# Kernel tuning notes

Measured on AMD Instinct MI355X. Metric: run time of the kernel, lower is better.

## Reference

```python
import jax, jax.numpy as jnp
import numpy as np

B, S, I, H = 32, 1024, 256, 256
NUM_LAYERS = 2


def _lstm_dir(x, m, h0, c0, Wih, Whh, bih, bhh, reverse=False):
    """x: [S,B,in], m: [S,B,1]. Returns outs [S,B,H], hT, cT.
    PyTorch LSTMCell gate order: i, f, g, o. Masked reset to init state per step."""
    if reverse:
        x = x[::-1]
        m = m[::-1]

    def step(carry, xm):
        h, c = carry
        xt, mt = xm
        gates = xt @ Wih.T + bih + h @ Whh.T + bhh  # [B,4H]
        i, f, g, o = jnp.split(gates, 4, axis=-1)
        i = jax.nn.sigmoid(i)
        f = jax.nn.sigmoid(f)
        g = jnp.tanh(g)
        o = jax.nn.sigmoid(o)
        cn = f * c + i * g
        hn = o * jnp.tanh(cn)
        hn = hn * mt + h0 * (1.0 - mt)
        cn = cn * mt + c0 * (1.0 - mt)
        return (hn, cn), hn

    (hT, cT), outs = jax.lax.scan(step, (h0, c0), (x, m))
    if reverse:
        outs = outs[::-1]
    return outs, hT, cT


def setup_inputs() -> dict:
    key = jax.random.key(0)
    ks = iter(jax.random.split(key, 40))
    d = {
        "inputs": jax.random.normal(next(ks), (B, S, I), dtype=jnp.float32),
        "mask": jnp.ones((B, S), dtype=jnp.float32),
    }
    scale = 0.05
    for li in range(NUM_LAYERS):
        in_sz = I if li == 0 else 2 * H
        for d_tag in ("f", "b"):
            p = f"l{li}{d_tag}_"
            d[p + "Wih"] = jax.random.normal(next(ks), (4 * H, in_sz), dtype=jnp.float32) * scale
            d[p + "Whh"] = jax.random.normal(next(ks), (4 * H, H), dtype=jnp.float32) * scale
            d[p + "bih"] = jnp.zeros((4 * H,), dtype=jnp.float32)
            d[p + "bhh"] = jnp.zeros((4 * H,), dtype=jnp.float32)
    return d


def reference(inputs, mask,
              l0f_Wih, l0f_Whh, l0f_bih, l0f_bhh,
              l0b_Wih, l0b_Whh, l0b_bih, l0b_bhh,
              l1f_Wih, l1f_Whh, l1f_bih, l1f_bhh,
              l1b_Wih, l1b_Whh, l1b_bih, l1b_bhh):
    # batch_first -> time-major
    x = jnp.transpose(inputs, (1, 0, 2))          # [S,B,I]
    m = jnp.transpose(mask, (1, 0))[:, :, None]   # [S,B,1] broadcasts over H
    h0 = jnp.zeros((B, H), dtype=inputs.dtype)
    c0 = h0

    layers = [
        ((l0f_Wih, l0f_Whh, l0f_bih, l0f_bhh), (l0b_Wih, l0b_Whh, l0b_bih, l0b_bhh)),
        ((l1f_Wih, l1f_Whh, l1f_bih, l1f_bhh), (l1b_Wih, l1b_Whh, l1b_bih, l1b_bhh)),
    ]
    hn, cn = [], []
    for fw_p, bw_p in layers:
        # (dropout between layers only active in training mode; eval reference skips it)
        fw_out, fh, fc = _lstm_dir(x, m, h0, c0, *fw_p, reverse=False)
        bw_out, bh, bc = _lstm_dir(x, m, h0, c0, *bw_p, reverse=True)
        x = jnp.concatenate((fw_out, bw_out), axis=2)  # [S,B,2H]
        hn.append(jnp.concatenate((fh, bh), axis=1))
        cn.append(jnp.concatenate((fc, bc), axis=1))

    output = jnp.transpose(x, (1, 0, 2))  # [B,S,2H]
    return output, jnp.stack(hn, axis=0), jnp.stack(cn, axis=0)
```

## Files before the change

### kernel.cpp

```cpp
#include <hip/hip_runtime.h>
#include <cstddef>

typedef __attribute__((ext_vector_type(8))) short short8;
typedef __attribute__((ext_vector_type(4))) short short4v;
typedef __attribute__((ext_vector_type(4))) float f32x4;

__device__ __forceinline__ unsigned short f2bf(float f){
  unsigned u = __builtin_bit_cast(unsigned, f);
  u += 0x7FFFu + ((u >> 16) & 1u);
  return (unsigned short)(u >> 16);
}
__device__ __forceinline__ float bf2f(unsigned short h){
  unsigned u = ((unsigned)h) << 16;
  return __builtin_bit_cast(float, u);
}
__device__ __forceinline__ float sigf(float x){
  return __builtin_amdgcn_rcpf(1.0f + __builtin_amdgcn_exp2f(-1.4426950408889634f * x));
}
__device__ __forceinline__ float tanhf_(float x){
  return 1.0f - 2.0f * __builtin_amdgcn_rcpf(1.0f + __builtin_amdgcn_exp2f(2.8853900817779268f * x));
}

__global__ __launch_bounds__(64) void cast_x(const float* __restrict__ in, unsigned short* __restrict__ xb){
  int blk = blockIdx.x;
  int t = blk & 1023, b = blk >> 10;
  int k = threadIdx.x * 4;
  float4 v = *(const float4*)(in + (size_t)blk * 256 + k);
  unsigned lo = f2bf(v.x) | ((unsigned)f2bf(v.y) << 16);
  unsigned hi = f2bf(v.z) | ((unsigned)f2bf(v.w) << 16);
  *(uint2*)(xb + ((size_t)t * 32 + b) * 256 + k) = make_uint2(lo, hi);
}

__global__ __launch_bounds__(64) void cast_w(const float* __restrict__ Wf, const float* __restrict__ Wb,
    const float* __restrict__ bihf, const float* __restrict__ bhhf,
    const float* __restrict__ bihb, const float* __restrict__ bhhb,
    unsigned short* __restrict__ Bw, float* __restrict__ bias, int K){
  int row = blockIdx.x;
  int dd = row >> 10, gc = row & 1023;
  const float* src = (dd ? Wb : Wf) + (size_t)gc * K;
  unsigned short* dst = Bw + (size_t)row * K;
  for (int k = threadIdx.x * 4; k < K; k += 256){
    float4 v = *(const float4*)(src + k);
    unsigned lo = f2bf(v.x) | ((unsigned)f2bf(v.y) << 16);
    unsigned hi = f2bf(v.z) | ((unsigned)f2bf(v.w) << 16);
    *(uint2*)(dst + k) = make_uint2(lo, hi);
  }
  if (threadIdx.x == 0)
    bias[row] = dd ? (bihb[gc] + bhhb[gc]) : (bihf[gc] + bhhf[gc]);
}

__global__ __launch_bounds__(256) void gemm_xg(const unsigned short* __restrict__ A,
    const unsigned short* __restrict__ Bw, const float* __restrict__ bias,
    unsigned short* __restrict__ xg, int K){
  __shared__ __align__(16) unsigned short Al[128 * 64];
  __shared__ __align__(16) unsigned short Bl[128 * 64];
  const int tid = threadIdx.x;
  const int w = tid >> 6, l = tid & 63, q = l >> 4, cl = l & 15;
  const int bm = blockIdx.x >> 4, bn = blockIdx.x & 15;
  const int wm = w & 1, wn = w >> 1;
  f32x4 acc[4][4];
#pragma unroll
  for (int nt = 0; nt < 4; ++nt){
    float bv = bias[bn * 128 + wn * 64 + nt * 16 + cl];
#pragma unroll
    for (int mt = 0; mt < 4; ++mt) acc[mt][nt] = (f32x4){bv, bv, bv, bv};
  }
  const unsigned short* Ab = A + (size_t)(bm * 128) * K;
  const unsigned short* Bb = Bw + (size_t)(bn * 128) * K;
  for (int k0 = 0; k0 < K; k0 += 64){
#pragma unroll
    for (int i = 0; i < 4; ++i){
      int task = tid + i * 256;
      int row = task >> 3, ch = task & 7;
      int sw = ((ch ^ (row & 7)) * 8);
      *(uint4*)(&Al[row * 64 + sw]) = *(const uint4*)(Ab + (size_t)row * K + k0 + ch * 8);
      *(uint4*)(&Bl[row * 64 + sw]) = *(const uint4*)(Bb + (size_t)row * K + k0 + ch * 8);
    }
    __syncthreads();
#pragma unroll
    for (int kt2 = 0; kt2 < 2; ++kt2){
      short8 af[4], bfv[4];
#pragma unroll
      for (int mt = 0; mt < 4; ++mt){
        int row = wm * 64 + mt * 16 + cl;
        af[mt] = *(const short8*)(&Al[row * 64 + (((kt2 * 4 + q) ^ (row & 7)) * 8)]);
      }
#pragma unroll
      for (int nt = 0; nt < 4; ++nt){
        int n = wn * 64 + nt * 16 + cl;
        bfv[nt] = *(const short8*)(&Bl[n * 64 + (((kt2 * 4 + q) ^ (n & 7)) * 8)]);
      }
#pragma unroll
      for (int mt = 0; mt < 4; ++mt)
#pragma unroll
        for (int nt = 0; nt < 4; ++nt)
          acc[mt][nt] = __builtin_amdgcn_mfma_f32_16x16x32_bf16(af[mt], bfv[nt], acc[mt][nt], 0, 0, 0);
    }
    __syncthreads();
  }
#pragma unroll
  for (int mt = 0; mt < 4; ++mt){
    int row = bm * 128 + wm * 64 + mt * 16 + q * 4;
    int tt = row >> 5, bb = row & 31;
#pragma unroll
    for (int nt = 0; nt < 4; ++nt){
      int col = bn * 128 + wn * 64 + nt * 16 + cl;
      f32x4 v = acc[mt][nt];
      unsigned lo = f2bf(v[0]) | ((unsigned)f2bf(v[1]) << 16);
      unsigned hi = f2bf(v[2]) | ((unsigned)f2bf(v[3]) << 16);
      *(uint2*)(xg + ((size_t)tt * 2048 + col) * 32 + bb) = make_uint2(lo, hi);
    }
  }
}

__global__ __launch_bounds__(256, 1) void lstm_rec(const unsigned short* __restrict__ xg,
    const float* __restrict__ WhhF, const float* __restrict__ WhhB,
    const float* __restrict__ mask, unsigned* __restrict__ hx,
    unsigned short* __restrict__ houts, float* __restrict__ out,
    float* __restrict__ hnout, float* __restrict__ cnout, int layer){
  __shared__ __align__(16) unsigned short Abuf[2 * 8 * 8 * 40];
  __shared__ float maskL[8192];
  const int tid = threadIdx.x;
  const int w = tid >> 6, l = tid & 63, q = l >> 4, cl = l & 15;
  const int u = blockIdx.x & 7, s = blockIdx.x >> 3;
  const int d = u >> 2, b0 = (u & 3) * 8;
  const float* __restrict__ Whh = d ? WhhB : WhhF;
  const int jj = s * 64 + w * 16 + cl;
  short8 bfrag[4][8];
#pragma unroll
  for (int gi = 0; gi < 4; ++gi){
    const float* wr = Whh + (size_t)(gi * 256 + jj) * 256 + q * 8;
#pragma unroll
    for (int kt = 0; kt < 8; ++kt){
      float4 x0 = *(const float4*)(wr + kt * 32);
      float4 x1 = *(const float4*)(wr + kt * 32 + 4);
      short8 f;
      f[0] = (short)f2bf(x0.x); f[1] = (short)f2bf(x0.y); f[2] = (short)f2bf(x0.z); f[3] = (short)f2bf(x0.w);
      f[4] = (short)f2bf(x1.x); f[5] = (short)f2bf(x1.y); f[6] = (short)f2bf(x1.z); f[7] = (short)f2bf(x1.w);
      bfrag[gi][kt] = f;
    }
  }
  for (int idx = tid; idx < 8192; idx += 256){
    int tt = idx >> 3, r = idx & 7;
    maskL[idx] = mask[(size_t)(b0 + r) * 1024 + tt];
  }
  __syncthreads();
  float cst[4] = {0.f, 0.f, 0.f, 0.f};
  unsigned* hxu = hx + (size_t)u * 4096;
  const bool qv = (q < 2);
  const int bq = b0 + q * 4;
  const int row8 = cl & 7;
  for (int t = 0; t < 1024; ++t){
    const int ot = d ? (1023 - t) : t;
    const int par = t & 1;
    f32x4 acc[4];
    if (qv){
#pragma unroll
      for (int gi = 0; gi < 4; ++gi){
        const unsigned short* xp = xg + ((size_t)ot * 2048 + (d * 1024 + gi * 256 + jj)) * 32 + bq;
        short4v xv = *(const short4v*)xp;
        acc[gi] = (f32x4){bf2f((unsigned short)xv[0]), bf2f((unsigned short)xv[1]),
                          bf2f((unsigned short)xv[2]), bf2f((unsigned short)xv[3])};
      }
    } else {
#pragma unroll
      for (int gi = 0; gi < 4; ++gi) acc[gi] = (f32x4){0.f, 0.f, 0.f, 0.f};
    }
    if (t > 0 && cl < 8){
      const unsigned* base = hxu + (size_t)(par ^ 1) * 2048 + cl * 256 + q * 8;
      const uint4* p0 = (const uint4*)(base + w * 32);
      const uint4* p1 = p0 + 1;
      const uint4* p2 = (const uint4*)(base + (w + 4) * 32);
      const uint4* p3 = p2 + 1;
      const unsigned tagv = (unsigned)t;
      uint4 va, vb, vc, vd;
      while (true){
        asm volatile(
          "global_load_dwordx4 %0, %4, off sc1\n\t"
          "global_load_dwordx4 %1, %5, off sc1\n\t"
          "global_load_dwordx4 %2, %6, off sc1\n\t"
          "global_load_dwordx4 %3, %7, off sc1\n\t"
          "s_waitcnt vmcnt(0)"
          : "=v"(va), "=v"(vb), "=v"(vc), "=v"(vd)
          : "v"(p0), "v"(p1), "v"(p2), "v"(p3)
          : "memory");
        unsigned x = (va.x ^ tagv) | (va.y ^ tagv) | (va.z ^ tagv) | (va.w ^ tagv)
                   | (vb.x ^ tagv) | (vb.y ^ tagv) | (vb.z ^ tagv) | (vb.w ^ tagv)
                   | (vc.x ^ tagv) | (vc.y ^ tagv) | (vc.z ^ tagv) | (vc.w ^ tagv)
                   | (vd.x ^ tagv) | (vd.y ^ tagv) | (vd.z ^ tagv) | (vd.w ^ tagv);
        if (__all((x & 0xFFFFu) == 0u)) break;
      }
      unsigned short* dst = &Abuf[par * 2560 + w * 320 + cl * 40 + q * 8];
      *(uint4*)dst = (uint4){ (va.x >> 16) | (va.y & 0xFFFF0000u), (va.z >> 16) | (va.w & 0xFFFF0000u),
                              (vb.x >> 16) | (vb.y & 0xFFFF0000u), (vb.z >> 16) | (vb.w & 0xFFFF0000u) };
      unsigned short* dst2 = &Abuf[par * 2560 + (w + 4) * 320 + cl * 40 + q * 8];
      *(uint4*)dst2 = (uint4){ (vc.x >> 16) | (vc.y & 0xFFFF0000u), (vc.z >> 16) | (vc.w & 0xFFFF0000u),
                               (vd.x >> 16) | (vd.y & 0xFFFF0000u), (vd.z >> 16) | (vd.w & 0xFFFF0000u) };
    }
    __syncthreads();
    if (t > 0){
      short8 af[8];
#pragma unroll
      for (int kt = 0; kt < 8; ++kt)
        af[kt] = *(const short8*)(&Abuf[par * 2560 + kt * 320 + row8 * 40 + q * 8]);
#pragma unroll
      for (int kt = 0; kt < 8; ++kt)
#pragma unroll
        for (int gi = 0; gi < 4; ++gi)
          acc[gi] = __builtin_amdgcn_mfma_f32_16x16x32_bf16(af[kt], bfrag[gi][kt], acc[gi], 0, 0, 0);
    }
    if (qv){
      float hv[4];
      unsigned short hb[4];
#pragma unroll
      for (int r = 0; r < 4; ++r){
        float mvr = maskL[ot * 8 + q * 4 + r];
        float ig = sigf(acc[0][r]);
        float fg = sigf(acc[1][r]);
        float gg = tanhf_(acc[2][r]);
        float og = sigf(acc[3][r]);
        float cn = fg * cst[r] + ig * gg;
        float hn = og * tanhf_(cn);
        hn *= mvr; cn *= mvr;
        cst[r] = cn; hv[r] = hn; hb[r] = f2bf(hn);
      }
      const unsigned tagn = (unsigned)(t + 1);
      unsigned* sw = hxu + (size_t)par * 2048 + (size_t)(q * 4) * 256 + jj;
#pragma unroll
      for (int r = 0; r < 4; ++r)
        __hip_atomic_store(sw + r * 256, ((unsigned)hb[r] << 16) | tagn,
                           __ATOMIC_RELAXED, __HIP_MEMORY_SCOPE_AGENT);
      if (layer == 0){
#pragma unroll
        for (int r = 0; r < 4; ++r)
          houts[((size_t)ot * 32 + bq + r) * 512 + d * 256 + jj] = hb[r];
      } else {
#pragma unroll
        for (int r = 0; r < 4; ++r)
          out[((size_t)(bq + r) * 1024 + ot) * 512 + d * 256 + jj] = hv[r];
      }
      if (t == 1023){
#pragma unroll
        for (int r = 0; r < 4; ++r){
          size_t bo = (size_t)(layer * 32 + bq + r) * 512 + d * 256 + jj;
          hnout[bo] = hv[r];
          cnout[bo] = cst[r];
        }
      }
    }
  }
}

extern "C" void kernel_launch(void* const* d_in, const int* in_sizes, int n_in,
                              void* d_out, int out_size, void* d_ws, size_t ws_size,
                              hipStream_t stream){
  const float* inputs  = (const float*)d_in[0];
  const float* mask    = (const float*)d_in[1];
  const float* l0f_Wih = (const float*)d_in[2];
  const float* l0f_Whh = (const float*)d_in[3];
  const float* l0f_bih = (const float*)d_in[4];
  const float* l0f_bhh = (const float*)d_in[5];
  const float* l0b_Wih = (const float*)d_in[6];
  const float* l0b_Whh = (const float*)d_in[7];
  const float* l0b_bih = (const float*)d_in[8];
  const float* l0b_bhh = (const float*)d_in[9];
  const float* l1f_Wih = (const float*)d_in[10];
  const float* l1f_Whh = (const float*)d_in[11];
  const float* l1f_bih = (const float*)d_in[12];
  const float* l1f_bhh = (const float*)d_in[13];
  const float* l1b_Wih = (const float*)d_in[14];
  const float* l1b_Whh = (const float*)d_in[15];
  const float* l1b_bih = (const float*)d_in[16];
  const float* l1b_bhh = (const float*)d_in[17];

  char* ws = (char*)d_ws;
  unsigned short* xg   = (unsigned short*)(ws);
  unsigned short* xbf  = (unsigned short*)(ws + 134217728);
  unsigned short* hout = (unsigned short*)(ws + 150994944);
  unsigned short* B0   = (unsigned short*)(ws + 184549376);
  unsigned short* B1   = (unsigned short*)(ws + 185597952);
  float* bias0         = (float*)(ws + 187695104);
  float* bias1         = (float*)(ws + 187703296);
  unsigned* hx         = (unsigned*)(ws + 187711488);

  float* out   = (float*)d_out;
  float* hnout = out + 16777216;
  float* cnout = hnout + 32768;

  hipMemsetAsync(hx, 0, 262144, stream);
  cast_x<<<32768, 64, 0, stream>>>(inputs, xbf);
  cast_w<<<2048, 64, 0, stream>>>(l0f_Wih, l0b_Wih, l0f_bih, l0f_bhh, l0b_bih, l0b_bhh, B0, bias0, 256);
  cast_w<<<2048, 64, 0, stream>>>(l1f_Wih, l1b_Wih, l1f_bih, l1f_bhh, l1b_bih, l1b_bhh, B1, bias1, 512);
  gemm_xg<<<4096, 256, 0, stream>>>(xbf, B0, bias0, xg, 256);
  lstm_rec<<<32, 256, 0, stream>>>(xg, l0f_Whh, l0b_Whh, mask, hx, hout, nullptr, hnout, cnout, 0);
  gemm_xg<<<4096, 256, 0, stream>>>(hout, B1, bias1, xg, 512);
  lstm_rec<<<32, 256, 0, stream>>>(xg, l1f_Whh, l1b_Whh, mask, hx + 32768, nullptr, out, hnout, cnout, 1);
}
```

Baseline: 4.087 ms.

## Load h directly into MFMA fragments per wave, dropping LDS staging and barrier

Result: slower. 7.316 ms (+79.0%).

```diff
diff --git a/kernel.cpp b/kernel.cpp
--- a/kernel.cpp
+++ b/kernel.cpp
@@ -4,6 +4,7 @@
 typedef __attribute__((ext_vector_type(8))) short short8;
 typedef __attribute__((ext_vector_type(4))) short short4v;
 typedef __attribute__((ext_vector_type(4))) float f32x4;
+typedef __attribute__((ext_vector_type(2))) unsigned short u16x2;
 
 __device__ __forceinline__ unsigned short f2bf(float f){
   unsigned u = __builtin_bit_cast(unsigned, f);
@@ -19,6 +20,12 @@
 }
 __device__ __forceinline__ float tanhf_(float x){
   return 1.0f - 2.0f * __builtin_amdgcn_rcpf(1.0f + __builtin_amdgcn_exp2f(2.8853900817779268f * x));
+}
+__device__ __forceinline__ u16x2 min4(uint4 a){
+  u16x2 x = __builtin_bit_cast(u16x2, a.x), y = __builtin_bit_cast(u16x2, a.y);
+  u16x2 z = __builtin_bit_cast(u16x2, a.z), w = __builtin_bit_cast(u16x2, a.w);
+  return __builtin_elementwise_min(__builtin_elementwise_min(x, y),
+                                   __builtin_elementwise_min(z, w));
 }
 
 __global__ __launch_bounds__(64) void cast_x(const float* __restrict__ in, unsigned short* __restrict__ xb){
@@ -118,7 +125,6 @@
     const float* __restrict__ mask, unsigned* __restrict__ hx,
     unsigned short* __restrict__ houts, float* __restrict__ out,
     float* __restrict__ hnout, float* __restrict__ cnout, int layer){
-  __shared__ __align__(16) unsigned short Abuf[2 * 8 * 8 * 40];
   __shared__ float maskL[8192];
   const int tid = threadIdx.x;
   const int w = tid >> 6, l = tid & 63, q = l >> 4, cl = l & 15;
@@ -149,7 +155,6 @@
   unsigned* hxu = hx + (size_t)u * 4096;
   const bool qv = (q < 2);
   const int bq = b0 + q * 4;
-  const int row8 = cl & 7;
   for (int t = 0; t < 1024; ++t){
     const int ot = d ? (1023 - t) : t;
     const int par = t & 1;
@@ -166,43 +171,64 @@
 #pragma unroll
       for (int gi = 0; gi < 4; ++gi) acc[gi] = (f32x4){0.f, 0.f, 0.f, 0.f};
     }
-    if (t > 0 && cl < 8){
-      const unsigned* base = hxu + (size_t)(par ^ 1) * 2048 + cl * 256 + q * 8;
-      const uint4* p0 = (const uint4*)(base + w * 32);
-      const uint4* p1 = p0 + 1;
-      const uint4* p2 = (const uint4*)(base + (w + 4) * 32);
-      const uint4* p3 = p2 + 1;
-      const unsigned tagv = (unsigned)t;
-      uint4 va, vb, vc, vd;
+    if (t > 0){
+      const unsigned* base = hxu + (size_t)(par ^ 1) * 2048 + (size_t)(cl & 7) * 256 + q * 8;
+      const unsigned short tagv = (unsigned short)t;
+      uint4 g0,g1,g2,g3,g4,g5,g6,g7,g8,g9,g10,g11,g12,g13,g14,g15;
       while (true){
         asm volatile(
-          "global_load_dwordx4 %0, %4, off sc1\n\t"
-          "global_load_dwordx4 %1, %5, off sc1\n\t"
-          "global_load_dwordx4 %2, %6, off sc1\n\t"
-          "global_load_dwordx4 %3, %7, off sc1\n\t"
+          "global_load_dwordx4 %0, %16, off sc1\n\t"
+          "global_load_dwordx4 %1, %16, off offset:16 sc1\n\t"
+          "global_load_dwordx4 %2, %16, off offset:128 sc1\n\t"
+          "global_load_dwordx4 %3, %16, off offset:144 sc1\n\t"
+          "global_load_dwordx4 %4, %16, off offset:256 sc1\n\t"
+          "global_load_dwordx4 %5, %16, off offset:272 sc1\n\t"
+          "global_load_dwordx4 %6, %16, off offset:384 sc1\n\t"
+          "global_load_dwordx4 %7, %16, off offset:400 sc1\n\t"
+          "global_load_dwordx4 %8, %16, off offset:512 sc1\n\t"
+          "global_load_dwordx4 %9, %16, off offset:528 sc1\n\t"
+          "global_load_dwordx4 %10, %16, off offset:640 sc1\n\t"
+          "global_load_dwordx4 %11, %16, off offset:656 sc1\n\t"
+          "global_load_dwordx4 %12, %16, off offset:768 sc1\n\t"
+          "global_load_dwordx4 %13, %16, off offset:784 sc1\n\t"
+          "global_load_dwordx4 %14, %16, off offset:896 sc1\n\t"
+          "global_load_dwordx4 %15, %16, off offset:912 sc1\n\t"
           "s_waitcnt vmcnt(0)"
-          : "=v"(va), "=v"(vb), "=v"(vc), "=v"(vd)
-          : "v"(p0), "v"(p1), "v"(p2), "v"(p3)
+          : "=v"(g0),"=v"(g1),"=v"(g2),"=v"(g3),"=v"(g4),"=v"(g5),"=v"(g6),"=v"(g7),
+            "=v"(g8),"=v"(g9),"=v"(g10),"=v"(g11),"=v"(g12),"=v"(g13),"=v"(g14),"=v"(g15)
+          : "v"(base)
           : "memory");
-        unsigned x = (va.x ^ tagv) | (va.y ^ tagv) | (va.z ^ tagv) | (va.w ^ tagv)
-                   | (vb.x ^ tagv) | (vb.y ^ tagv) | (vb.z ^ tagv) | (vb.w ^ tagv)
-                   | (vc.x ^ tagv) | (vc.y ^ tagv) | (vc.z ^ tagv) | (vc.w ^ tagv)
-                   | (vd.x ^ tagv) | (vd.y ^ tagv) | (vd.z ^ tagv) | (vd.w ^ tagv);
-        if (__all((x & 0xFFFFu) == 0u)) break;
-      }
-      unsigned short* dst = &Abuf[par * 2560 + w * 320 + cl * 40 + q * 8];
-      *(uint4*)dst = (uint4){ (va.x >> 16) | (va.y & 0xFFFF0000u), (va.z >> 16) | (va.w & 0xFFFF0000u),
-                              (vb.x >> 16) | (vb.y & 0xFFFF0000u), (vb.z >> 16) | (vb.w & 0xFFFF0000u) };
-      unsigned short* dst2 = &Abuf[par * 2560 + (w + 4) * 320 + cl * 40 + q * 8];
-      *(uint4*)dst2 = (uint4){ (vc.x >> 16) | (vc.y & 0xFFFF0000u), (vc.z >> 16) | (vc.w & 0xFFFF0000u),
-                               (vd.x >> 16) | (vd.y & 0xFFFF0000u), (vd.z >> 16) | (vd.w & 0xFFFF0000u) };
-    }
-    __syncthreads();
-    if (t > 0){
+        u16x2 m = __builtin_elementwise_min(
+          __builtin_elementwise_min(
+            __builtin_elementwise_min(__builtin_elementwise_min(min4(g0), min4(g1)),
+                                      __builtin_elementwise_min(min4(g2), min4(g3))),
+            __builtin_elementwise_min(__builtin_elementwise_min(min4(g4), min4(g5)),
+                                      __builtin_elementwise_min(min4(g6), min4(g7)))),
+          __builtin_elementwise_min(
+            __builtin_elementwise_min(__builtin_elementwise_min(min4(g8), min4(g9)),
+                                      __builtin_elementwise_min(min4(g10), min4(g11))),
+            __builtin_elementwise_min(__builtin_elementwise_min(min4(g12), min4(g13)),
+                                      __builtin_elementwise_min(min4(g14), min4(g15)))));
+        if (__all(m[0] >= tagv)) break;
+      }
+      uint4 ga[8] = { (uint4){g0.x,g0.y,g0.z,g0.w}, (uint4){g2.x,g2.y,g2.z,g2.w},
+                      (uint4){g4.x,g4.y,g4.z,g4.w}, (uint4){g6.x,g6.y,g6.z,g6.w},
+                      (uint4){g8.x,g8.y,g8.z,g8.w}, (uint4){g10.x,g10.y,g10.z,g10.w},
+                      (uint4){g12.x,g12.y,g12.z,g12.w}, (uint4){g14.x,g14.y,g14.z,g14.w} };
+      uint4 gb[8] = { (uint4){g1.x,g1.y,g1.z,g1.w}, (uint4){g3.x,g3.y,g3.z,g3.w},
+                      (uint4){g5.x,g5.y,g5.z,g5.w}, (uint4){g7.x,g7.y,g7.z,g7.w},
+                      (uint4){g9.x,g9.y,g9.z,g9.w}, (uint4){g11.x,g11.y,g11.z,g11.w},
+                      (uint4){g13.x,g13.y,g13.z,g13.w}, (uint4){g15.x,g15.y,g15.z,g15.w} };
       short8 af[8];
 #pragma unroll
-      for (int kt = 0; kt < 8; ++kt)
-        af[kt] = *(const short8*)(&Abuf[par * 2560 + kt * 320 + row8 * 40 + q * 8]);
+      for (int kt = 0; kt < 8; ++kt){
+        uint4 p;
+        p.x = (ga[kt].x >> 16) | (ga[kt].y & 0xFFFF0000u);
+        p.y = (ga[kt].z >> 16) | (ga[kt].w & 0xFFFF0000u);
+        p.z = (gb[kt].x >> 16) | (gb[kt].y & 0xFFFF0000u);
+        p.w = (gb[kt].z >> 16) | (gb[kt].w & 0xFFFF0000u);
+        af[kt] = __builtin_bit_cast(short8, p);
+      }
 #pragma unroll
       for (int kt = 0; kt < 8; ++kt)
 #pragma unroll
```

## Replace block barrier with LDS wave flags and min-tag polling in LSTM recurrence

Applied to the files above, without the earlier changes.

Result: slower. 4.497 ms (+10.0%).

```diff
diff --git a/kernel.cpp b/kernel.cpp
--- a/kernel.cpp
+++ b/kernel.cpp
@@ -4,6 +4,7 @@
 typedef __attribute__((ext_vector_type(8))) short short8;
 typedef __attribute__((ext_vector_type(4))) short short4v;
 typedef __attribute__((ext_vector_type(4))) float f32x4;
+typedef __attribute__((ext_vector_type(2))) unsigned short u16x2;
 
 __device__ __forceinline__ unsigned short f2bf(float f){
   unsigned u = __builtin_bit_cast(unsigned, f);
@@ -19,6 +20,12 @@
 }
 __device__ __forceinline__ float tanhf_(float x){
   return 1.0f - 2.0f * __builtin_amdgcn_rcpf(1.0f + __builtin_amdgcn_exp2f(2.8853900817779268f * x));
+}
+__device__ __forceinline__ u16x2 min4(uint4 a){
+  u16x2 x = __builtin_bit_cast(u16x2, a.x), y = __builtin_bit_cast(u16x2, a.y);
+  u16x2 z = __builtin_bit_cast(u16x2, a.z), w = __builtin_bit_cast(u16x2, a.w);
+  return __builtin_elementwise_min(__builtin_elementwise_min(x, y),
+                                   __builtin_elementwise_min(z, w));
 }
 
 __global__ __launch_bounds__(64) void cast_x(const float* __restrict__ in, unsigned short* __restrict__ xb){
@@ -118,8 +125,9 @@
     const float* __restrict__ mask, unsigned* __restrict__ hx,
     unsigned short* __restrict__ houts, float* __restrict__ out,
     float* __restrict__ hnout, float* __restrict__ cnout, int layer){
-  __shared__ __align__(16) unsigned short Abuf[2 * 8 * 8 * 40];
   __shared__ float maskL[8192];
+  __shared__ __align__(16) unsigned char AbufB[2 * 5120];
+  __shared__ int lflag[8];
   const int tid = threadIdx.x;
   const int w = tid >> 6, l = tid & 63, q = l >> 4, cl = l & 15;
   const int u = blockIdx.x & 7, s = blockIdx.x >> 3;
@@ -140,6 +148,7 @@
       bfrag[gi][kt] = f;
     }
   }
+  if (tid < 8) lflag[tid] = 0;
   for (int idx = tid; idx < 8192; idx += 256){
     int tt = idx >> 3, r = idx & 7;
     maskL[idx] = mask[(size_t)(b0 + r) * 1024 + tt];
@@ -166,43 +175,51 @@
 #pragma unroll
       for (int gi = 0; gi < 4; ++gi) acc[gi] = (f32x4){0.f, 0.f, 0.f, 0.f};
     }
-    if (t > 0 && cl < 8){
-      const unsigned* base = hxu + (size_t)(par ^ 1) * 2048 + cl * 256 + q * 8;
-      const uint4* p0 = (const uint4*)(base + w * 32);
-      const uint4* p1 = p0 + 1;
-      const uint4* p2 = (const uint4*)(base + (w + 4) * 32);
-      const uint4* p3 = p2 + 1;
-      const unsigned tagv = (unsigned)t;
-      uint4 va, vb, vc, vd;
-      while (true){
-        asm volatile(
-          "global_load_dwordx4 %0, %4, off sc1\n\t"
-          "global_load_dwordx4 %1, %5, off sc1\n\t"
-          "global_load_dwordx4 %2, %6, off sc1\n\t"
-          "global_load_dwordx4 %3, %7, off sc1\n\t"
-          "s_waitcnt vmcnt(0)"
-          : "=v"(va), "=v"(vb), "=v"(vc), "=v"(vd)
-          : "v"(p0), "v"(p1), "v"(p2), "v"(p3)
-          : "memory");
-        unsigned x = (va.x ^ tagv) | (va.y ^ tagv) | (va.z ^ tagv) | (va.w ^ tagv)
-                   | (vb.x ^ tagv) | (vb.y ^ tagv) | (vb.z ^ tagv) | (vb.w ^ tagv)
-                   | (vc.x ^ tagv) | (vc.y ^ tagv) | (vc.z ^ tagv) | (vc.w ^ tagv)
-                   | (vd.x ^ tagv) | (vd.y ^ tagv) | (vd.z ^ tagv) | (vd.w ^ tagv);
-        if (__all((x & 0xFFFFu) == 0u)) break;
-      }
-      unsigned short* dst = &Abuf[par * 2560 + w * 320 + cl * 40 + q * 8];
-      *(uint4*)dst = (uint4){ (va.x >> 16) | (va.y & 0xFFFF0000u), (va.z >> 16) | (va.w & 0xFFFF0000u),
-                              (vb.x >> 16) | (vb.y & 0xFFFF0000u), (vb.z >> 16) | (vb.w & 0xFFFF0000u) };
-      unsigned short* dst2 = &Abuf[par * 2560 + (w + 4) * 320 + cl * 40 + q * 8];
-      *(uint4*)dst2 = (uint4){ (vc.x >> 16) | (vc.y & 0xFFFF0000u), (vc.z >> 16) | (vc.w & 0xFFFF0000u),
-                               (vd.x >> 16) | (vd.y & 0xFFFF0000u), (vd.z >> 16) | (vd.w & 0xFFFF0000u) };
-    }
-    __syncthreads();
     if (t > 0){
+      if (cl < 8){
+        const unsigned* base = hxu + (size_t)(par ^ 1) * 2048 + (size_t)row8 * 256 + q * 8 + w * 64;
+        const unsigned short tagv = (unsigned short)t;
+        uint4 ga, gb, gc, gd;
+        int guard = 0;
+        while (true){
+          asm volatile(
+            "global_load_dwordx4 %0, %4, off sc1\n\t"
+            "global_load_dwordx4 %1, %4, off offset:16 sc1\n\t"
+            "global_load_dwordx4 %2, %4, off offset:128 sc1\n\t"
+            "global_load_dwordx4 %3, %4, off offset:144 sc1\n\t"
+            "s_waitcnt vmcnt(0)"
+            : "=&v"(ga), "=&v"(gb), "=&v"(gc), "=&v"(gd)
+            : "v"(base)
+            : "memory");
+          u16x2 m = __builtin_elementwise_min(__builtin_elementwise_min(min4(ga), min4(gb)),
+                                              __builtin_elementwise_min(min4(gc), min4(gd)));
+          if (__all(m[0] >= tagv)) break;
+          if (++guard > (1 << 20)) break;
+          __builtin_amdgcn_s_sleep(1);
+        }
+        uint4 p0, p1;
+        p0.x = (ga.x >> 16) | (ga.y & 0xFFFF0000u); p0.y = (ga.z >> 16) | (ga.w & 0xFFFF0000u);
+        p0.z = (gb.x >> 16) | (gb.y & 0xFFFF0000u); p0.w = (gb.z >> 16) | (gb.w & 0xFFFF0000u);
+        p1.x = (gc.x >> 16) | (gc.y & 0xFFFF0000u); p1.y = (gc.z >> 16) | (gc.w & 0xFFFF0000u);
+        p1.z = (gd.x >> 16) | (gd.y & 0xFFFF0000u); p1.w = (gd.z >> 16) | (gd.w & 0xFFFF0000u);
+        *(uint4*)(&AbufB[par * 5120 + (2 * w) * 640 + row8 * 80 + q * 16]) = p0;
+        *(uint4*)(&AbufB[par * 5120 + (2 * w + 1) * 640 + row8 * 80 + q * 16]) = p1;
+      }
+      asm volatile("s_waitcnt lgkmcnt(0)" ::: "memory");
+      if (l == 0)
+        ((volatile int*)lflag)[par * 4 + w] = t;
+      {
+        volatile int* vf = (volatile int*)lflag + par * 4;
+        int guard = 0;
+        while (vf[0] < t || vf[1] < t || vf[2] < t || vf[3] < t){
+          if (++guard > (1 << 24)) break;
+        }
+      }
+      asm volatile("" ::: "memory");
       short8 af[8];
 #pragma unroll
       for (int kt = 0; kt < 8; ++kt)
-        af[kt] = *(const short8*)(&Abuf[par * 2560 + kt * 320 + row8 * 40 + q * 8]);
+        af[kt] = *(const short8*)(&AbufB[par * 5120 + kt * 640 + row8 * 80 + q * 16]);
 #pragma unroll
       for (int kt = 0; kt < 8; ++kt)
 #pragma unroll
```
